# Kernel tuning notes

Measured on AMD Instinct MI355X. Metric: run time of the kernel, lower is better.

## Reference

```python
import jax, jax.numpy as jnp
import numpy as np

N, E, DIN, DH, DOUT = 100000, 600000, 128, 128, 64


def _glorot(k, shape):
    lim = float(np.sqrt(6.0 / (shape[0] + shape[1])))
    return jax.random.uniform(k, shape, jnp.float32, -lim, lim)


def setup_inputs() -> dict:
    key = jax.random.key(0)
    ks = jax.random.split(key, 12)
    return {
        "x": jax.random.normal(ks[0], (N, DIN), jnp.float32),
        "src": jax.random.randint(ks[1], (E,), 0, N),
        "dst": jax.random.randint(ks[2], (E,), 0, N),
        # layer 0: NGNN_SAGEConv = SAGEConv(in,hid) + fc(hid,hid) + fc2(hid,hid)
        "w_self0": _glorot(ks[3], (DIN, DH)), "b_self0": jnp.zeros((DH,), jnp.float32),
        "w_neigh0": _glorot(ks[4], (DIN, DH)),
        "fc_w": _glorot(ks[5], (DH, DH)), "fc_b": jnp.zeros((DH,), jnp.float32),
        "fc2_w": _glorot(ks[6], (DH, DH)), "fc2_b": jnp.zeros((DH,), jnp.float32),
        # layer 1: SAGEConv(hid,hid)
        "w_self1": _glorot(ks[7], (DH, DH)), "b_self1": jnp.zeros((DH,), jnp.float32),
        "w_neigh1": _glorot(ks[8], (DH, DH)),
        # layer 2: SAGEConv(hid,out)
        "w_self2": _glorot(ks[9], (DH, DOUT)), "b_self2": jnp.zeros((DOUT,), jnp.float32),
        "w_neigh2": _glorot(ks[10], (DH, DOUT)),
    }


def _sage_conv(x, src, dst, w_self, b_self, w_neigh):
    # DGL SAGEConv, aggregator='mean': out = x @ W_self + b + mean_{u->v} x_u @ W_neigh
    agg = jax.ops.segment_sum(x[src], dst, num_segments=N)          # [N, d_in]
    deg = jax.ops.segment_sum(jnp.ones((src.shape[0],), x.dtype), dst, num_segments=N)
    h_neigh = agg / jnp.maximum(deg, 1.0)[:, None]                  # zero-in-degree -> 0
    return x @ w_self + b_self + h_neigh @ w_neigh


def reference(x, src, dst,
              w_self0, b_self0, w_neigh0, fc_w, fc_b, fc2_w, fc2_b,
              w_self1, b_self1, w_neigh1,
              w_self2, b_self2, w_neigh2):
    # layer 0: NGNN_SAGEConv with num_nonl_layers=2, then outer ReLU (dropout: eval = identity)
    h = _sage_conv(x, src, dst, w_self0, b_self0, w_neigh0)
    h = jax.nn.relu(h)
    h = h @ fc_w + fc_b
    h = jax.nn.relu(h)
    h = h @ fc2_w + fc2_b
    h = jax.nn.relu(h)
    # layer 1: SAGEConv + ReLU
    h = _sage_conv(h, src, dst, w_self1, b_self1, w_neigh1)
    h = jax.nn.relu(h)
    # layer 2 (output): SAGEConv, no activation
    return _sage_conv(h, src, dst, w_self2, b_self2, w_neigh2)
```

## Files before the change

kernel.cpp:

```cpp
#include <hip/hip_runtime.h>

#define N_NODES 100000
#define N_EDGES 600000
#define K_DIM   128
#define NPART   ((N_NODES + 255) / 256)

typedef unsigned short ushort_t;
typedef short v8s __attribute__((ext_vector_type(8)));
typedef float v4f __attribute__((ext_vector_type(4)));

__device__ __forceinline__ ushort_t f2b(float f) {
  unsigned u = __builtin_bit_cast(unsigned, f);
  unsigned r = u + 0x7FFFu + ((u >> 16) & 1u);
  return (ushort_t)(r >> 16);
}
__device__ __forceinline__ float b2f(ushort_t h) {
  return __builtin_bit_cast(float, (unsigned)h << 16);
}
__device__ __forceinline__ float blo(unsigned u) {
  return __builtin_bit_cast(float, u << 16);
}
__device__ __forceinline__ float bhi(unsigned u) {
  return __builtin_bit_cast(float, u & 0xFFFF0000u);
}


__global__ void deg_kernel(const int* __restrict__ dst, int* __restrict__ deg) {
  int e = blockIdx.x * blockDim.x + threadIdx.x;
  if (e < N_EDGES) atomicAdd(&deg[dst[e]], 1);
}

__global__ void scan1_kernel(const int* __restrict__ deg, int* __restrict__ excl,
                             int* __restrict__ partials) {
  __shared__ int s[256];
  int t = threadIdx.x, i = blockIdx.x * 256 + t;
  int v = (i < N_NODES) ? deg[i] : 0;
  s[t] = v;
  __syncthreads();
  for (int off = 1; off < 256; off <<= 1) {
    int x = (t >= off) ? s[t - off] : 0;
    __syncthreads();
    s[t] += x;
    __syncthreads();
  }
  if (i < N_NODES) excl[i] = s[t] - v;
  if (t == 255) partials[blockIdx.x] = s[t];
}

__global__ void scan2_kernel(int* __restrict__ partials) {
  __shared__ int s[512];
  int t = threadIdx.x;
  int v = (t < NPART) ? partials[t] : 0;
  s[t] = v;
  __syncthreads();
  for (int off = 1; off < 512; off <<= 1) {
    int x = (t >= off) ? s[t - off] : 0;
    __syncthreads();
    s[t] += x;
    __syncthreads();
  }
  if (t < NPART) partials[t] = s[t] - v;
}

__global__ void scan3_kernel(const int* __restrict__ excl, const int* __restrict__ partials,
                             const int* __restrict__ deg, int* __restrict__ row_ptr,
                             int* __restrict__ cursor, float* __restrict__ inv_deg) {
  int i = blockIdx.x * blockDim.x + threadIdx.x;
  if (i < N_NODES) {
    int rp = excl[i] + partials[i >> 8];
    row_ptr[i] = rp;
    cursor[i] = rp;
    inv_deg[i] = 1.0f / (float)(deg[i] > 1 ? deg[i] : 1);
  } else if (i == N_NODES) {
    row_ptr[N_NODES] = N_EDGES;
  }
}

__global__ void fill_kernel(const int* __restrict__ src, const int* __restrict__ dst,
                            int* __restrict__ cursor, int* __restrict__ ssrc) {
  int e = blockIdx.x * blockDim.x + threadIdx.x;
  if (e < N_EDGES) {
    int p = atomicAdd(&cursor[dst[e]], 1);
    ssrc[p] = src[e];
  }
}


__global__ void cast_kernel(const float* __restrict__ X, ushort_t* __restrict__ Xb) {
  int i = (blockIdx.x * 256 + threadIdx.x) * 8;
  if (i >= N_NODES * K_DIM) return;
  float4 v0 = *(const float4*)(X + i);
  float4 v1 = *(const float4*)(X + i + 4);
  ushort4 h0, h1;
  h0.x = f2b(v0.x); h0.y = f2b(v0.y); h0.z = f2b(v0.z); h0.w = f2b(v0.w);
  h1.x = f2b(v1.x); h1.y = f2b(v1.y); h1.z = f2b(v1.z); h1.w = f2b(v1.w);
  *(ushort4*)(Xb + i)     = h0;
  *(ushort4*)(Xb + i + 4) = h1;
}

__global__ void swizzle_all_kernel(
    const float* __restrict__ w0, const float* __restrict__ w1,
    const float* __restrict__ w2, const float* __restrict__ w3,
    const float* __restrict__ w4, const float* __restrict__ w5,
    const float* __restrict__ w6, const float* __restrict__ w7,
    ushort_t* __restrict__ s0, ushort_t* __restrict__ s1,
    ushort_t* __restrict__ s2, ushort_t* __restrict__ s3,
    ushort_t* __restrict__ s4, ushort_t* __restrict__ s5,
    ushort_t* __restrict__ s6, ushort_t* __restrict__ s7) {
  const int z = blockIdx.z;
  const float* W;
  ushort_t* S;
  int dout = 128;
  switch (z) {
    case 0: W = w0; S = s0; break;
    case 1: W = w1; S = s1; break;
    case 2: W = w2; S = s2; break;
    case 3: W = w3; S = s3; break;
    case 4: W = w4; S = s4; break;
    case 5: W = w5; S = s5; break;
    case 6: W = w6; S = s6; dout = 64; break;
    default: W = w7; S = s7; dout = 64; break;
  }
  int t = blockIdx.x * 256 + threadIdx.x;
  if (t >= K_DIM * dout) return;
  int k = t / dout, n = t % dout;
  S[(k >> 3) * (dout * 8) + n * 8 + (k & 7)] = f2b(W[t]);
}


__global__ __launch_bounds__(256, 8) void agg_kernel(
    const ushort_t* __restrict__ Hh,
    const int* __restrict__ row_ptr, const int* __restrict__ ssrc,
    const float* __restrict__ inv_deg, ushort_t* __restrict__ Ah) {
  const int tid = threadIdx.x;
  const int c0  = (tid & 15) * 8;
  const int r   = tid >> 4;
  const int v   = blockIdx.x * 16 + r;
  if (v >= N_NODES) return;

  float a[8];
  #pragma unroll
  for (int i = 0; i < 8; ++i) a[i] = 0.f;

  const int beg = row_ptr[v], end = row_ptr[v + 1];
  int e = beg;
  for (; e + 4 <= end; e += 4) {
    const int s0 = ssrc[e];
    const int s1 = ssrc[e + 1];
    const int s2 = ssrc[e + 2];
    const int s3 = ssrc[e + 3];
    const uint4 p0 = *(const uint4*)(Hh + (size_t)s0 * K_DIM + c0);
    const uint4 p1 = *(const uint4*)(Hh + (size_t)s1 * K_DIM + c0);
    const uint4 p2 = *(const uint4*)(Hh + (size_t)s2 * K_DIM + c0);
    const uint4 p3 = *(const uint4*)(Hh + (size_t)s3 * K_DIM + c0);
    a[0] += (blo(p0.x) + blo(p1.x)) + (blo(p2.x) + blo(p3.x));
    a[1] += (bhi(p0.x) + bhi(p1.x)) + (bhi(p2.x) + bhi(p3.x));
    a[2] += (blo(p0.y) + blo(p1.y)) + (blo(p2.y) + blo(p3.y));
    a[3] += (bhi(p0.y) + bhi(p1.y)) + (bhi(p2.y) + bhi(p3.y));
    a[4] += (blo(p0.z) + blo(p1.z)) + (blo(p2.z) + blo(p3.z));
    a[5] += (bhi(p0.z) + bhi(p1.z)) + (bhi(p2.z) + bhi(p3.z));
    a[6] += (blo(p0.w) + blo(p1.w)) + (blo(p2.w) + blo(p3.w));
    a[7] += (bhi(p0.w) + bhi(p1.w)) + (bhi(p2.w) + bhi(p3.w));
  }
  if (e + 2 <= end) {
    const int s0 = ssrc[e];
    const int s1 = ssrc[e + 1];
    const uint4 p0 = *(const uint4*)(Hh + (size_t)s0 * K_DIM + c0);
    const uint4 p1 = *(const uint4*)(Hh + (size_t)s1 * K_DIM + c0);
    a[0] += blo(p0.x) + blo(p1.x);
    a[1] += bhi(p0.x) + bhi(p1.x);
    a[2] += blo(p0.y) + blo(p1.y);
    a[3] += bhi(p0.y) + bhi(p1.y);
    a[4] += blo(p0.z) + blo(p1.z);
    a[5] += bhi(p0.z) + bhi(p1.z);
    a[6] += blo(p0.w) + blo(p1.w);
    a[7] += bhi(p0.w) + bhi(p1.w);
    e += 2;
  }
  if (e < end) {
    const int s0 = ssrc[e];
    const uint4 p0 = *(const uint4*)(Hh + (size_t)s0 * K_DIM + c0);
    a[0] += blo(p0.x);
    a[1] += bhi(p0.x);
    a[2] += blo(p0.y);
    a[3] += bhi(p0.y);
    a[4] += blo(p0.z);
    a[5] += bhi(p0.z);
    a[6] += blo(p0.w);
    a[7] += bhi(p0.w);
  }
  const float sc = inv_deg[v];
  ushort4 o0, o1;
  o0.x = f2b(a[0] * sc); o0.y = f2b(a[1] * sc);
  o0.z = f2b(a[2] * sc); o0.w = f2b(a[3] * sc);
  o1.x = f2b(a[4] * sc); o1.y = f2b(a[5] * sc);
  o1.z = f2b(a[6] * sc); o1.w = f2b(a[7] * sc);
  const size_t wo = (size_t)v * K_DIM + c0;
  *(ushort4*)(Ah + wo)     = o0;
  *(ushort4*)(Ah + wo + 4) = o1;
}


template <int DOUT_FULL, bool TWO, bool RELU, bool BF16_OUT>
__global__ __launch_bounds__(256, 4) void mfma_gemm_kernel(
    const ushort_t* __restrict__ A1, const ushort_t* __restrict__ A2,
    const ushort_t* __restrict__ W1sw, const ushort_t* __restrict__ W2sw,
    const float* __restrict__ bias,
    ushort_t* __restrict__ Obf, float* __restrict__ Ofp) {
  constexpr int COLT = 64;
  constexpr int NT   = COLT / 16;
  constexpr int SWN  = (K_DIM / 8) * COLT * 8;
  __shared__ ushort_t sW[SWN];

  const int tid  = threadIdx.x;
  const int wv   = tid >> 6;
  const int lane = tid & 63;
  const int lm   = lane & 15;
  const int q    = lane >> 4;
  const int row0 = blockIdx.x * 128 + wv * 32;
  const int col0 = blockIdx.y * COLT;

  for (int i = tid * 8; i < SWN; i += 2048) {
    const int kg = i / (COLT * 8);
    const int nl = (i >> 3) & (COLT - 1);
    *(uint4*)&sW[i] = *(const uint4*)&W1sw[kg * (DOUT_FULL * 8) + (col0 + nl) * 8];
  }
  __syncthreads();

  int ra = row0 + lm;       ra = ra < N_NODES ? ra : N_NODES - 1;
  int rb = row0 + 16 + lm;  rb = rb < N_NODES ? rb : N_NODES - 1;
  const size_t off0 = (size_t)ra * K_DIM;
  const size_t off1 = (size_t)rb * K_DIM;

  v4f acc[2][NT];
  #pragma unroll
  for (int m = 0; m < 2; ++m)
    #pragma unroll
    for (int n = 0; n < NT; ++n) acc[m][n] = (v4f){0.f, 0.f, 0.f, 0.f};

  for (int ks = 0; ks < K_DIM / 32; ++ks) {
    const int ko = ks * 32 + q * 8;
    const v8s a0 = *(const v8s*)(A1 + off0 + ko);
    const v8s a1 = *(const v8s*)(A1 + off1 + ko);
    #pragma unroll
    for (int nt = 0; nt < NT; ++nt) {
      const v8s b = *(const v8s*)&sW[((ks * 4 + q) * COLT + nt * 16 + lm) * 8];
      acc[0][nt] = __builtin_amdgcn_mfma_f32_16x16x32_bf16(a0, b, acc[0][nt], 0, 0, 0);
      acc[1][nt] = __builtin_amdgcn_mfma_f32_16x16x32_bf16(a1, b, acc[1][nt], 0, 0, 0);
    }
  }

  if (TWO) {
    __syncthreads();
    for (int i = tid * 8; i < SWN; i += 2048) {
      const int kg = i / (COLT * 8);
      const int nl = (i >> 3) & (COLT - 1);
      *(uint4*)&sW[i] = *(const uint4*)&W2sw[kg * (DOUT_FULL * 8) + (col0 + nl) * 8];
    }
    __syncthreads();

    for (int ks = 0; ks < K_DIM / 32; ++ks) {
      const int ko = ks * 32 + q * 8;
      const v8s a0 = *(const v8s*)(A2 + off0 + ko);
      const v8s a1 = *(const v8s*)(A2 + off1 + ko);
      #pragma unroll
      for (int nt = 0; nt < NT; ++nt) {
        const v8s b = *(const v8s*)&sW[((ks * 4 + q) * COLT + nt * 16 + lm) * 8];
        acc[0][nt] = __builtin_amdgcn_mfma_f32_16x16x32_bf16(a0, b, acc[0][nt], 0, 0, 0);
        acc[1][nt] = __builtin_amdgcn_mfma_f32_16x16x32_bf16(a1, b, acc[1][nt], 0, 0, 0);
      }
    }
  }

  #pragma unroll
  for (int m = 0; m < 2; ++m) {
    #pragma unroll
    for (int nt = 0; nt < NT; ++nt) {
      const int col = col0 + nt * 16 + lm;
      const float bv = bias[col];
      #pragma unroll
      for (int r = 0; r < 4; ++r) {
        const int row = row0 + m * 16 + q * 4 + r;
        if (row < N_NODES) {
          float v = acc[m][nt][r] + bv;
          if (RELU) v = v > 0.f ? v : 0.f;
          if (BF16_OUT) Obf[(size_t)row * DOUT_FULL + col] = f2b(v);
          else          Ofp[(size_t)row * DOUT_FULL + col] = v;
        }
      }
    }
  }
}


__global__ __launch_bounds__(512, 4) void fused_fc_kernel(
    const ushort_t* __restrict__ A,
    const ushort_t* __restrict__ W1sw, const ushort_t* __restrict__ W2sw,
    const float* __restrict__ b1, const float* __restrict__ b2,
    ushort_t* __restrict__ O) {
  constexpr int NT = 8;
  constexpr int HP = 136;
  __shared__ ushort_t bufW[K_DIM * 128];
  __shared__ ushort_t bufH[128 * HP];

  const int tid   = threadIdx.x;
  const int wv    = tid >> 6;
  const int lane  = tid & 63;
  const int lm    = lane & 15;
  const int q     = lane >> 4;
  const int lrow0 = wv * 16;
  const int row0  = blockIdx.x * 128 + lrow0;

  for (int i = tid * 8; i < K_DIM * 128; i += 4096)
    *(uint4*)&bufW[i] = *(const uint4*)&W1sw[i];

  uint4 wreg[4];
  #pragma unroll
  for (int j = 0; j < 4; ++j)
    wreg[j] = *(const uint4*)&W2sw[tid * 8 + j * 4096];

  __syncthreads();

  int ra = row0 + lm;  ra = ra < N_NODES ? ra : N_NODES - 1;
  const size_t off0 = (size_t)ra * K_DIM;

  v4f acc[NT];
  #pragma unroll
  for (int n = 0; n < NT; ++n) acc[n] = (v4f){0.f, 0.f, 0.f, 0.f};

  for (int ks = 0; ks < K_DIM / 32; ++ks) {
    const int ko = ks * 32 + q * 8;
    const v8s a0 = *(const v8s*)(A + off0 + ko);
    #pragma unroll
    for (int nt = 0; nt < NT; ++nt) {
      const v8s b = *(const v8s*)&bufW[((ks * 4 + q) * 128 + nt * 16 + lm) * 8];
      acc[nt] = __builtin_amdgcn_mfma_f32_16x16x32_bf16(a0, b, acc[nt], 0, 0, 0);
    }
  }
  __syncthreads();

  #pragma unroll
  for (int j = 0; j < 4; ++j)
    *(uint4*)&bufW[tid * 8 + j * 4096] = wreg[j];
  #pragma unroll
  for (int nt = 0; nt < NT; ++nt) {
    const int col = nt * 16 + lm;
    const float bv = b1[col];
    #pragma unroll
    for (int r = 0; r < 4; ++r) {
      float v = acc[nt][r] + bv;
      v = v > 0.f ? v : 0.f;
      bufH[(lrow0 + q * 4 + r) * HP + col] = f2b(v);
      acc[nt][r] = 0.f;
    }
  }
  __syncthreads();

  for (int ks = 0; ks < K_DIM / 32; ++ks) {
    const int ko = ks * 32 + q * 8;
    const v8s a0 = *(const v8s*)&bufH[(lrow0 + lm) * HP + ko];
    #pragma unroll
    for (int nt = 0; nt < NT; ++nt) {
      const v8s b = *(const v8s*)&bufW[((ks * 4 + q) * 128 + nt * 16 + lm) * 8];
      acc[nt] = __builtin_amdgcn_mfma_f32_16x16x32_bf16(a0, b, acc[nt], 0, 0, 0);
    }
  }

  #pragma unroll
  for (int nt = 0; nt < NT; ++nt) {
    const int col = nt * 16 + lm;
    const float bv = b2[col];
    #pragma unroll
    for (int r = 0; r < 4; ++r) {
      const int row = row0 + q * 4 + r;
      if (row < N_NODES) {
        float v = acc[nt][r] + bv;
        v = v > 0.f ? v : 0.f;
        O[(size_t)row * 128 + col] = f2b(v);
      }
    }
  }
}


extern "C" void kernel_launch(void* const* d_in, const int* in_sizes, int n_in,
                              void* d_out, int out_size, void* d_ws, size_t ws_size,
                              hipStream_t stream) {
  const float* x        = (const float*)d_in[0];
  const int*   src      = (const int*)d_in[1];
  const int*   dst      = (const int*)d_in[2];
  const float* w_self0  = (const float*)d_in[3];
  const float* b_self0  = (const float*)d_in[4];
  const float* w_neigh0 = (const float*)d_in[5];
  const float* fc_w     = (const float*)d_in[6];
  const float* fc_b     = (const float*)d_in[7];
  const float* fc2_w    = (const float*)d_in[8];
  const float* fc2_b    = (const float*)d_in[9];
  const float* w_self1  = (const float*)d_in[10];
  const float* b_self1  = (const float*)d_in[11];
  const float* w_neigh1 = (const float*)d_in[12];
  const float* w_self2  = (const float*)d_in[13];
  const float* b_self2  = (const float*)d_in[14];
  const float* w_neigh2 = (const float*)d_in[15];

  char* p = (char*)d_ws;
  auto carve = [&](size_t bytes) {
    void* q = (void*)p;
    p += (bytes + 511) & ~(size_t)511;
    return q;
  };
  const size_t PLANE = (size_t)N_NODES * K_DIM * sizeof(ushort_t);
  ushort_t* X   = (ushort_t*)carve(PLANE);
  ushort_t* Y   = (ushort_t*)carve(PLANE);
  ushort_t* Z   = (ushort_t*)carve(PLANE);
  ushort_t* ws0 = (ushort_t*)carve(K_DIM * 128 * 2);
  ushort_t* wn0 = (ushort_t*)carve(K_DIM * 128 * 2);
  ushort_t* wfc = (ushort_t*)carve(K_DIM * 128 * 2);
  ushort_t* wf2 = (ushort_t*)carve(K_DIM * 128 * 2);
  ushort_t* ws1 = (ushort_t*)carve(K_DIM * 128 * 2);
  ushort_t* wn1 = (ushort_t*)carve(K_DIM * 128 * 2);
  ushort_t* ws2 = (ushort_t*)carve(K_DIM * 64 * 2);
  ushort_t* wn2 = (ushort_t*)carve(K_DIM * 64 * 2);
  int*   ssrc    = (int*)carve((size_t)N_EDGES * 4);
  int*   row_ptr = (int*)carve((size_t)(N_NODES + 1) * 4);
  int*   cursor  = (int*)carve((size_t)N_NODES * 4);
  int*   deg     = (int*)carve((size_t)N_NODES * 4);
  int*   excl    = (int*)carve((size_t)N_NODES * 4);
  int*   parts   = (int*)carve(512 * 4);
  float* inv_deg = (float*)carve((size_t)N_NODES * 4);

  hipMemsetAsync(deg, 0, (size_t)N_NODES * 4, stream);
  const int EB = (N_EDGES + 255) / 256;
  deg_kernel<<<EB, 256, 0, stream>>>(dst, deg);
  scan1_kernel<<<NPART, 256, 0, stream>>>(deg, excl, parts);
  scan2_kernel<<<1, 512, 0, stream>>>(parts);
  scan3_kernel<<<((N_NODES + 1) + 255) / 256, 256, 0, stream>>>(excl, parts, deg,
                                                                row_ptr, cursor, inv_deg);
  fill_kernel<<<EB, 256, 0, stream>>>(src, dst, cursor, ssrc);

  cast_kernel<<<(N_NODES * K_DIM / 8 + 255) / 256, 256, 0, stream>>>(x, X);
  swizzle_all_kernel<<<dim3(64, 1, 8), 256, 0, stream>>>(
      w_self0, w_neigh0, fc_w, fc2_w, w_self1, w_neigh1, w_self2, w_neigh2,
      ws0, wn0, wfc, wf2, ws1, wn1, ws2, wn2);

  const int AB = (N_NODES + 15) / 16;
  const int GB = (N_NODES + 127) / 128;
  const dim3 G2(GB, 2), G1(GB, 1);

  agg_kernel<<<AB, 256, 0, stream>>>(X, row_ptr, ssrc, inv_deg, Y);
  mfma_gemm_kernel<128, true, true, true><<<G2, 256, 0, stream>>>(
      X, Y, ws0, wn0, b_self0, Z, nullptr);
  fused_fc_kernel<<<G1, 512, 0, stream>>>(Z, wfc, wf2, fc_b, fc2_b, Y);
  agg_kernel<<<AB, 256, 0, stream>>>(Y, row_ptr, ssrc, inv_deg, X);
  mfma_gemm_kernel<128, true, true, true><<<G2, 256, 0, stream>>>(
      Y, X, ws1, wn1, b_self1, Z, nullptr);
  agg_kernel<<<AB, 256, 0, stream>>>(Z, row_ptr, ssrc, inv_deg, Y);
  mfma_gemm_kernel<64, true, false, false><<<G1, 256, 0, stream>>>(
      Z, Y, ws2, wn2, b_self2, nullptr, (float*)d_out);
}
```

Before: 371.2 us.

## Restructure SAGE GEMM to full-width tiles and merge setup kernels

The dual-input SAGE GEMM now uses 512-thread blocks that cover the full output width, so each A row is read once instead of once per 64-column half. The second weight matrix is prefetched into registers while the first GEMM pass runs. The degree count is merged with the input cast, and the scan1 step with the weight swizzle, which removes two kernel launches. In exchange each wave now computes 16 rows instead of 32, which gives fewer MFMAs per A load, and the larger LDS footprint may lower occupancy.

```diff
diff --git a/kernel.cpp b/kernel.cpp
--- a/kernel.cpp
+++ b/kernel.cpp
@@ -4,6 +4,8 @@
 #define N_EDGES 600000
 #define K_DIM   128
 #define NPART   ((N_NODES + 255) / 256)
+#define EBLK    ((N_EDGES + 255) / 256)
+#define CASTB   (N_NODES * K_DIM / 8 / 256)
 
 typedef unsigned short ushort_t;
 typedef short v8s __attribute__((ext_vector_type(8)));
@@ -25,26 +27,69 @@
 }
 
 
-__global__ void deg_kernel(const int* __restrict__ dst, int* __restrict__ deg) {
-  int e = blockIdx.x * blockDim.x + threadIdx.x;
-  if (e < N_EDGES) atomicAdd(&deg[dst[e]], 1);
-}
-
-__global__ void scan1_kernel(const int* __restrict__ deg, int* __restrict__ excl,
-                             int* __restrict__ partials) {
+__global__ void deg_cast_kernel(const int* __restrict__ dst, int* __restrict__ deg,
+                                const float* __restrict__ X, ushort_t* __restrict__ Xb) {
+  if (blockIdx.x < EBLK) {
+    int e = blockIdx.x * 256 + threadIdx.x;
+    if (e < N_EDGES) atomicAdd(&deg[dst[e]], 1);
+  } else {
+    int i = ((blockIdx.x - EBLK) * 256 + threadIdx.x) * 8;
+    if (i >= N_NODES * K_DIM) return;
+    float4 v0 = *(const float4*)(X + i);
+    float4 v1 = *(const float4*)(X + i + 4);
+    ushort4 h0, h1;
+    h0.x = f2b(v0.x); h0.y = f2b(v0.y); h0.z = f2b(v0.z); h0.w = f2b(v0.w);
+    h1.x = f2b(v1.x); h1.y = f2b(v1.y); h1.z = f2b(v1.z); h1.w = f2b(v1.w);
+    *(ushort4*)(Xb + i)     = h0;
+    *(ushort4*)(Xb + i + 4) = h1;
+  }
+}
+
+__global__ void scan1_swz_kernel(
+    const int* __restrict__ deg, int* __restrict__ excl, int* __restrict__ partials,
+    const float* __restrict__ w0, const float* __restrict__ w1,
+    const float* __restrict__ w2, const float* __restrict__ w3,
+    const float* __restrict__ w4, const float* __restrict__ w5,
+    const float* __restrict__ w6, const float* __restrict__ w7,
+    ushort_t* __restrict__ s0, ushort_t* __restrict__ s1,
+    ushort_t* __restrict__ s2, ushort_t* __restrict__ s3,
+    ushort_t* __restrict__ s4, ushort_t* __restrict__ s5,
+    ushort_t* __restrict__ s6, ushort_t* __restrict__ s7) {
   __shared__ int s[256];
-  int t = threadIdx.x, i = blockIdx.x * 256 + t;
-  int v = (i < N_NODES) ? deg[i] : 0;
-  s[t] = v;
-  __syncthreads();
-  for (int off = 1; off < 256; off <<= 1) {
-    int x = (t >= off) ? s[t - off] : 0;
+  if (blockIdx.x < NPART) {
+    int t = threadIdx.x, i = blockIdx.x * 256 + t;
+    int v = (i < N_NODES) ? deg[i] : 0;
+    s[t] = v;
     __syncthreads();
-    s[t] += x;
-    __syncthreads();
-  }
-  if (i < N_NODES) excl[i] = s[t] - v;
-  if (t == 255) partials[blockIdx.x] = s[t];
+    for (int off = 1; off < 256; off <<= 1) {
+      int x = (t >= off) ? s[t - off] : 0;
+      __syncthreads();
+      s[t] += x;
+      __syncthreads();
+    }
+    if (i < N_NODES) excl[i] = s[t] - v;
+    if (t == 255) partials[blockIdx.x] = s[t];
+  } else {
+    const int blk = blockIdx.x - NPART;
+    const int z = blk >> 6;
+    const float* W;
+    ushort_t* S;
+    int dout = 128;
+    switch (z) {
+      case 0: W = w0; S = s0; break;
+      case 1: W = w1; S = s1; break;
+      case 2: W = w2; S = s2; break;
+      case 3: W = w3; S = s3; break;
+      case 4: W = w4; S = s4; break;
+      case 5: W = w5; S = s5; break;
+      case 6: W = w6; S = s6; dout = 64; break;
+      default: W = w7; S = s7; dout = 64; break;
+    }
+    int t = (blk & 63) * 256 + threadIdx.x;
+    if (t >= K_DIM * dout) return;
+    int k = t / dout, n = t % dout;
+    S[(k >> 3) * (dout * 8) + n * 8 + (k & 7)] = f2b(W[t]);
+  }
 }
 
 __global__ void scan2_kernel(int* __restrict__ partials) {
@@ -83,48 +128,6 @@
     int p = atomicAdd(&cursor[dst[e]], 1);
     ssrc[p] = src[e];
   }
-}
-
-
-__global__ void cast_kernel(const float* __restrict__ X, ushort_t* __restrict__ Xb) {
-  int i = (blockIdx.x * 256 + threadIdx.x) * 8;
-  if (i >= N_NODES * K_DIM) return;
-  float4 v0 = *(const float4*)(X + i);
-  float4 v1 = *(const float4*)(X + i + 4);
-  ushort4 h0, h1;
-  h0.x = f2b(v0.x); h0.y = f2b(v0.y); h0.z = f2b(v0.z); h0.w = f2b(v0.w);
-  h1.x = f2b(v1.x); h1.y = f2b(v1.y); h1.z = f2b(v1.z); h1.w = f2b(v1.w);
-  *(ushort4*)(Xb + i)     = h0;
-  *(ushort4*)(Xb + i + 4) = h1;
-}
-
-__global__ void swizzle_all_kernel(
-    const float* __restrict__ w0, const float* __restrict__ w1,
-    const float* __restrict__ w2, const float* __restrict__ w3,
-    const float* __restrict__ w4, const float* __restrict__ w5,
-    const float* __restrict__ w6, const float* __restrict__ w7,
-    ushort_t* __restrict__ s0, ushort_t* __restrict__ s1,
-    ushort_t* __restrict__ s2, ushort_t* __restrict__ s3,
-    ushort_t* __restrict__ s4, ushort_t* __restrict__ s5,
-    ushort_t* __restrict__ s6, ushort_t* __restrict__ s7) {
-  const int z = blockIdx.z;
-  const float* W;
-  ushort_t* S;
-  int dout = 128;
-  switch (z) {
-    case 0: W = w0; S = s0; break;
-    case 1: W = w1; S = s1; break;
-    case 2: W = w2; S = s2; break;
-    case 3: W = w3; S = s3; break;
-    case 4: W = w4; S = s4; break;
-    case 5: W = w5; S = s5; break;
-    case 6: W = w6; S = s6; dout = 64; break;
-    default: W = w7; S = s7; dout = 64; break;
-  }
-  int t = blockIdx.x * 256 + threadIdx.x;
-  if (t >= K_DIM * dout) return;
-  int k = t / dout, n = t % dout;
-  S[(k >> 3) * (dout * 8) + n * 8 + (k & 7)] = f2b(W[t]);
 }
 
 
@@ -201,92 +204,78 @@
 }
 
 
-template <int DOUT_FULL, bool TWO, bool RELU, bool BF16_OUT>
-__global__ __launch_bounds__(256, 4) void mfma_gemm_kernel(
+template <int DOUT, bool RELU, bool BF16_OUT>
+__global__ __launch_bounds__(512, 4) void mfma_gemm_kernel(
     const ushort_t* __restrict__ A1, const ushort_t* __restrict__ A2,
     const ushort_t* __restrict__ W1sw, const ushort_t* __restrict__ W2sw,
     const float* __restrict__ bias,
     ushort_t* __restrict__ Obf, float* __restrict__ Ofp) {
-  constexpr int COLT = 64;
-  constexpr int NT   = COLT / 16;
-  constexpr int SWN  = (K_DIM / 8) * COLT * 8;
-  __shared__ ushort_t sW[SWN];
-
-  const int tid  = threadIdx.x;
-  const int wv   = tid >> 6;
-  const int lane = tid & 63;
-  const int lm   = lane & 15;
-  const int q    = lane >> 4;
-  const int row0 = blockIdx.x * 128 + wv * 32;
-  const int col0 = blockIdx.y * COLT;
-
-  for (int i = tid * 8; i < SWN; i += 2048) {
-    const int kg = i / (COLT * 8);
-    const int nl = (i >> 3) & (COLT - 1);
-    *(uint4*)&sW[i] = *(const uint4*)&W1sw[kg * (DOUT_FULL * 8) + (col0 + nl) * 8];
-  }
-  __syncthreads();
-
-  int ra = row0 + lm;       ra = ra < N_NODES ? ra : N_NODES - 1;
-  int rb = row0 + 16 + lm;  rb = rb < N_NODES ? rb : N_NODES - 1;
+  constexpr int NT  = DOUT / 16;
+  constexpr int SWN = K_DIM * DOUT;
+  constexpr int NW  = SWN / 4096;
+  __shared__ ushort_t bufW[SWN];
+
+  const int tid   = threadIdx.x;
+  const int wv    = tid >> 6;
+  const int lane  = tid & 63;
+  const int lm    = lane & 15;
+  const int q     = lane >> 4;
+  const int row0  = blockIdx.x * 128 + wv * 16;
+
+  #pragma unroll
+  for (int j = 0; j < NW; ++j)
+    *(uint4*)&bufW[tid * 8 + j * 4096] = *(const uint4*)&W1sw[tid * 8 + j * 4096];
+  uint4 wreg[NW];
+  #pragma unroll
+  for (int j = 0; j < NW; ++j)
+    wreg[j] = *(const uint4*)&W2sw[tid * 8 + j * 4096];
+  __syncthreads();
+
+  int ra = row0 + lm;  ra = ra < N_NODES ? ra : N_NODES - 1;
   const size_t off0 = (size_t)ra * K_DIM;
-  const size_t off1 = (size_t)rb * K_DIM;
-
-  v4f acc[2][NT];
-  #pragma unroll
-  for (int m = 0; m < 2; ++m)
-    #pragma unroll
-    for (int n = 0; n < NT; ++n) acc[m][n] = (v4f){0.f, 0.f, 0.f, 0.f};
+
+  v4f acc[NT];
+  #pragma unroll
+  for (int n = 0; n < NT; ++n) acc[n] = (v4f){0.f, 0.f, 0.f, 0.f};
 
   for (int ks = 0; ks < K_DIM / 32; ++ks) {
     const int ko = ks * 32 + q * 8;
     const v8s a0 = *(const v8s*)(A1 + off0 + ko);
-    const v8s a1 = *(const v8s*)(A1 + off1 + ko);
     #pragma unroll
     for (int nt = 0; nt < NT; ++nt) {
-      const v8s b = *(const v8s*)&sW[((ks * 4 + q) * COLT + nt * 16 + lm) * 8];
-      acc[0][nt] = __builtin_amdgcn_mfma_f32_16x16x32_bf16(a0, b, acc[0][nt], 0, 0, 0);
-      acc[1][nt] = __builtin_amdgcn_mfma_f32_16x16x32_bf16(a1, b, acc[1][nt], 0, 0, 0);
-    }
-  }
-
-  if (TWO) {
-    __syncthreads();
-    for (int i = tid * 8; i < SWN; i += 2048) {
-      const int kg = i / (COLT * 8);
-      const int nl = (i >> 3) & (COLT - 1);
-      *(uint4*)&sW[i] = *(const uint4*)&W2sw[kg * (DOUT_FULL * 8) + (col0 + nl) * 8];
-    }
-    __syncthreads();
-
-    for (int ks = 0; ks < K_DIM / 32; ++ks) {
-      const int ko = ks * 32 + q * 8;
-      const v8s a0 = *(const v8s*)(A2 + off0 + ko);
-      const v8s a1 = *(const v8s*)(A2 + off1 + ko);
-      #pragma unroll
-      for (int nt = 0; nt < NT; ++nt) {
-        const v8s b = *(const v8s*)&sW[((ks * 4 + q) * COLT + nt * 16 + lm) * 8];
-        acc[0][nt] = __builtin_amdgcn_mfma_f32_16x16x32_bf16(a0, b, acc[0][nt], 0, 0, 0);
-        acc[1][nt] = __builtin_amdgcn_mfma_f32_16x16x32_bf16(a1, b, acc[1][nt], 0, 0, 0);
-      }
-    }
-  }
-
-  #pragma unroll
-  for (int m = 0; m < 2; ++m) {
+      const v8s b = *(const v8s*)&bufW[((ks * 4 + q) * DOUT + nt * 16 + lm) * 8];
+      acc[nt] = __builtin_amdgcn_mfma_f32_16x16x32_bf16(a0, b, acc[nt], 0, 0, 0);
+    }
+  }
+  __syncthreads();
+
+  #pragma unroll
+  for (int j = 0; j < NW; ++j)
+    *(uint4*)&bufW[tid * 8 + j * 4096] = wreg[j];
+  __syncthreads();
+
+  for (int ks = 0; ks < K_DIM / 32; ++ks) {
+    const int ko = ks * 32 + q * 8;
+    const v8s a0 = *(const v8s*)(A2 + off0 + ko);
     #pragma unroll
     for (int nt = 0; nt < NT; ++nt) {
-      const int col = col0 + nt * 16 + lm;
-      const float bv = bias[col];
-      #pragma unroll
-      for (int r = 0; r < 4; ++r) {
-        const int row = row0 + m * 16 + q * 4 + r;
-        if (row < N_NODES) {
-          float v = acc[m][nt][r] + bv;
-          if (RELU) v = v > 0.f ? v : 0.f;
-          if (BF16_OUT) Obf[(size_t)row * DOUT_FULL + col] = f2b(v);
-          else          Ofp[(size_t)row * DOUT_FULL + col] = v;
-        }
+      const v8s b = *(const v8s*)&bufW[((ks * 4 + q) * DOUT + nt * 16 + lm) * 8];
+      acc[nt] = __builtin_amdgcn_mfma_f32_16x16x32_bf16(a0, b, acc[nt], 0, 0, 0);
+    }
+  }
+
+  #pragma unroll
+  for (int nt = 0; nt < NT; ++nt) {
+    const int col = nt * 16 + lm;
+    const float bv = bias[col];
+    #pragma unroll
+    for (int r = 0; r < 4; ++r) {
+      const int row = row0 + q * 4 + r;
+      if (row < N_NODES) {
+        float v = acc[nt][r] + bv;
+        if (RELU) v = v > 0.f ? v : 0.f;
+        if (BF16_OUT) Obf[(size_t)row * DOUT + col] = f2b(v);
+        else          Ofp[(size_t)row * DOUT + col] = v;
       }
     }
   }
@@ -430,31 +419,27 @@
   float* inv_deg = (float*)carve((size_t)N_NODES * 4);
 
   hipMemsetAsync(deg, 0, (size_t)N_NODES * 4, stream);
-  const int EB = (N_EDGES + 255) / 256;
-  deg_kernel<<<EB, 256, 0, stream>>>(dst, deg);
-  scan1_kernel<<<NPART, 256, 0, stream>>>(deg, excl, parts);
+  deg_cast_kernel<<<EBLK + CASTB, 256, 0, stream>>>(dst, deg, x, X);
+  scan1_swz_kernel<<<NPART + 512, 256, 0, stream>>>(
+      deg, excl, parts,
+      w_self0, w_neigh0, fc_w, fc2_w, w_self1, w_neigh1, w_self2, w_neigh2,
+      ws0, wn0, wfc, wf2, ws1, wn1, ws2, wn2);
   scan2_kernel<<<1, 512, 0, stream>>>(parts);
   scan3_kernel<<<((N_NODES + 1) + 255) / 256, 256, 0, stream>>>(excl, parts, deg,
                                                                 row_ptr, cursor, inv_deg);
-  fill_kernel<<<EB, 256, 0, stream>>>(src, dst, cursor, ssrc);
-
-  cast_kernel<<<(N_NODES * K_DIM / 8 + 255) / 256, 256, 0, stream>>>(x, X);
-  swizzle_all_kernel<<<dim3(64, 1, 8), 256, 0, stream>>>(
-      w_self0, w_neigh0, fc_w, fc2_w, w_self1, w_neigh1, w_self2, w_neigh2,
-      ws0, wn0, wfc, wf2, ws1, wn1, ws2, wn2);
+  fill_kernel<<<EBLK, 256, 0, stream>>>(src, dst, cursor, ssrc);
 
   const int AB = (N_NODES + 15) / 16;
   const int GB = (N_NODES + 127) / 128;
-  const dim3 G2(GB, 2), G1(GB, 1);
 
   agg_kernel<<<AB, 256, 0, stream>>>(X, row_ptr, ssrc, inv_deg, Y);
-  mfma_gemm_kernel<128, true, true, true><<<G2, 256, 0, stream>>>(
+  mfma_gemm_kernel<128, true, true><<<GB, 512, 0, stream>>>(
       X, Y, ws0, wn0, b_self0, Z, nullptr);
-  fused_fc_kernel<<<G1, 512, 0, stream>>>(Z, wfc, wf2, fc_b, fc2_b, Y);
+  fused_fc_kernel<<<GB, 512, 0, stream>>>(Z, wfc, wf2, fc_b, fc2_b, Y);
   agg_kernel<<<AB, 256, 0, stream>>>(Y, row_ptr, ssrc, inv_deg, X);
-  mfma_gemm_kernel<128, true, true, true><<<G2, 256, 0, stream>>>(
+  mfma_gemm_kernel<128, true, true><<<GB, 512, 0, stream>>>(
       Y, X, ws1, wn1, b_self1, Z, nullptr);
   agg_kernel<<<AB, 256, 0, stream>>>(Z, row_ptr, ssrc, inv_deg, Y);
-  mfma_gemm_kernel<64, true, false, false><<<G1, 256, 0, stream>>>(
+  mfma_gemm_kernel<64, false, false><<<GB, 512, 0, stream>>>(
       Z, Y, ws2, wn2, b_self2, nullptr, (float*)d_out);
 }
```

After: 392.4 us. 5.7% more time.
